# Kernel tuning notes

Measured on AMD Instinct MI355X. Metric: run time of the kernel, lower is better.

## Reference

```python
import jax, jax.numpy as jnp
import numpy as np

NUM_OBJECTS = 32  # instance ids 1..32; id 0 = background (skipped in original loop)


def setup_inputs() -> dict:
    key = jax.random.key(0)
    k0, k1, k2, k3 = jax.random.split(key, 4)
    B, C, H, W = 4, 256, 256, 256
    encoded = jax.random.normal(k0, (B, C, H, W), dtype=jnp.float32)
    # dense random ids 0..NUM_OBJECTS; with 65536 pixels every id appears w.h.p.
    masks = jax.random.randint(k1, (B, 1, H, W), 0, NUM_OBJECTS + 1, dtype=jnp.int32)
    w1 = jax.random.normal(k2, (C, C // 2), dtype=jnp.float32) * 0.02
    b1 = jnp.zeros((C // 2,), dtype=jnp.float32)
    w2 = jax.random.normal(k3, (C // 2, 4), dtype=jnp.float32) * 0.02
    b2 = jnp.zeros((4,), dtype=jnp.float32)
    return {"encoded": encoded, "w1": w1, "b1": b1, "w2": w2, "b2": b2, "masks": masks}


def reference(encoded, w1, b1, w2, b2, masks):
    # encoded: [B, C, H, W], masks: [B, 1, H, W] int ids in [0, NUM_OBJECTS]
    B, C, H, W = encoded.shape
    P = H * W
    ids = masks[:, 0].reshape(B, P)                      # [B, P]
    feat = encoded.reshape(B, C, P).transpose(0, 2, 1)   # [B, P, C]
    # Fused single-pass segmented max (replaces the per-id rescan loop).
    seg = jax.vmap(
        lambda d, i: jax.ops.segment_max(d, i, num_segments=NUM_OBJECTS + 1)
    )(feat, ids)                                          # [B, N+1, C]
    # Original computes max(mask * feat): zeros outside the mask participate in
    # the max, so the result is clamped at 0. Also fills any empty segment with 0.
    pooled = jnp.maximum(seg[:, 1:], 0.0)                 # [B, N, C] (drop background id 0)
    h = pooled @ w1 + b1                                  # [B, N, C//2]
    bbox = jax.nn.sigmoid(h @ w2 + b2)                    # [B, N, 4]
    return bbox
```

## Files before the change

kernel.cpp:

```cpp
#include <hip/hip_runtime.h>
#include <math.h>

#define BATCH   4
#define CH      256
#define PIX     65536
#define NIDS    33
#define NOBJ    32

__global__ __launch_bounds__(256, 1) void segmax_kernel(
    const float* __restrict__ encoded,
    const int*   __restrict__ masks,
    float*       __restrict__ pooled)
{
    __shared__ float smax[NIDS * 256];
    __shared__ float partial[NOBJ * 8];

    const int t   = threadIdx.x;
    const int bid = blockIdx.x;
    const int b   = bid >> 8;
    const int c   = bid & 255;

    #pragma unroll
    for (int i = 0; i < NIDS; ++i)
        smax[i * 256 + t] = -INFINITY;
    __syncthreads();

    const float4* __restrict__ vals = (const float4*)(encoded + (size_t)bid * PIX);
    const int4*   __restrict__ ids  = (const int4*)(masks + (size_t)b * PIX);

    #pragma unroll 2
    for (int it = 0; it < 64; ++it) {
        const int idx = it * 256 + t;
        const float4 v = vals[idx];
        const int4   m = ids[idx];
        { float* p = &smax[m.x * 256 + t]; *p = fmaxf(*p, v.x); }
        { float* p = &smax[m.y * 256 + t]; *p = fmaxf(*p, v.y); }
        { float* p = &smax[m.z * 256 + t]; *p = fmaxf(*p, v.z); }
        { float* p = &smax[m.w * 256 + t]; *p = fmaxf(*p, v.w); }
    }
    __syncthreads();

    {
        const int id   = 1 + (t >> 3);
        const int g    = t & 7;
        const int base = id * 256 + g * 32;
        float m = -INFINITY;
        #pragma unroll
        for (int j = 0; j < 32; ++j) {
            const int jj = (j + t) & 31;
            m = fmaxf(m, smax[base + jj]);
        }
        partial[(id - 1) * 8 + g] = m;
    }
    __syncthreads();

    if (t < NOBJ) {
        float m = -INFINITY;
        #pragma unroll
        for (int g = 0; g < 8; ++g) m = fmaxf(m, partial[t * 8 + g]);
        m = fmaxf(m, 0.0f);
        pooled[((size_t)b * NOBJ + t) * CH + c] = m;
    }
}

__global__ __launch_bounds__(128, 1) void mlp_kernel(
    const float* __restrict__ pooled,
    const float* __restrict__ w1, const float* __restrict__ b1,
    const float* __restrict__ w2, const float* __restrict__ b2,
    float*       __restrict__ out)
{
    __shared__ float row[CH];
    __shared__ float h[128];
    const int t = threadIdx.x;
    const int r = blockIdx.x;

    row[t]       = pooled[(size_t)r * CH + t];
    row[t + 128] = pooled[(size_t)r * CH + t + 128];
    __syncthreads();

    float acc = b1[t];
    #pragma unroll 8
    for (int i = 0; i < CH; ++i)
        acc = fmaf(row[i], w1[i * 128 + t], acc);
    h[t] = acc;
    __syncthreads();

    if (t < 4) {
        float a = b2[t];
        #pragma unroll 8
        for (int i = 0; i < 128; ++i)
            a = fmaf(h[i], w2[i * 4 + t], a);
        out[(size_t)r * 4 + t] = 1.0f / (1.0f + expf(-a));
    }
}

extern "C" void kernel_launch(void* const* d_in, const int* in_sizes, int n_in,
                              void* d_out, int out_size, void* d_ws, size_t ws_size,
                              hipStream_t stream) {
    const float* encoded = (const float*)d_in[0];
    const float* w1      = (const float*)d_in[1];
    const float* b1      = (const float*)d_in[2];
    const float* w2      = (const float*)d_in[3];
    const float* b2      = (const float*)d_in[4];
    const int*   masks   = (const int*)  d_in[5];
    float* out    = (float*)d_out;
    float* pooled = (float*)d_ws;

    segmax_kernel<<<BATCH * CH, 256, 0, stream>>>(encoded, masks, pooled);
    mlp_kernel<<<BATCH * NOBJ, 128, 0, stream>>>(pooled, w1, b1, w2, b2, out);
}
```

Before: 384.8 us.

## Pack mask ids to bytes, split pixel range across two blocks, prefetch loads

```diff
diff --git a/kernel.cpp b/kernel.cpp
--- a/kernel.cpp
+++ b/kernel.cpp
@@ -6,37 +6,62 @@
 #define PIX     65536
 #define NIDS    33
 #define NOBJ    32
+#define SSPLIT  2
+#define F4_SLICE (PIX / 4)
+#define F4_PER_S (F4_SLICE / SSPLIT)
+#define ITERS    (F4_PER_S / 256)
+
+typedef float f32x4 __attribute__((ext_vector_type(4)));
+
+__global__ __launch_bounds__(256) void pack_masks_kernel(
+    const int* __restrict__ masks, unsigned int* __restrict__ maskw)
+{
+    const int idx = blockIdx.x * 256 + threadIdx.x;
+    const int4 v = ((const int4*)masks)[idx];
+    maskw[idx] = (unsigned)v.x | ((unsigned)v.y << 8) |
+                 ((unsigned)v.z << 16) | ((unsigned)v.w << 24);
+}
 
 __global__ __launch_bounds__(256, 1) void segmax_kernel(
-    const float* __restrict__ encoded,
-    const int*   __restrict__ masks,
-    float*       __restrict__ pooled)
+    const float*        __restrict__ encoded,
+    const unsigned int* __restrict__ maskw,
+    float*              __restrict__ pooledP)
 {
     __shared__ float smax[NIDS * 256];
     __shared__ float partial[NOBJ * 8];
 
-    const int t   = threadIdx.x;
-    const int bid = blockIdx.x;
-    const int b   = bid >> 8;
-    const int c   = bid & 255;
+    const int t     = threadIdx.x;
+    const int slice = blockIdx.x >> 1;
+    const int s     = blockIdx.x & 1;
+    const int b     = slice >> 8;
+    const int c     = slice & 255;
 
     #pragma unroll
     for (int i = 0; i < NIDS; ++i)
         smax[i * 256 + t] = -INFINITY;
     __syncthreads();
 
-    const float4* __restrict__ vals = (const float4*)(encoded + (size_t)bid * PIX);
-    const int4*   __restrict__ ids  = (const int4*)(masks + (size_t)b * PIX);
+    const f32x4* __restrict__ vals =
+        (const f32x4*)encoded + (size_t)slice * F4_SLICE + (size_t)s * F4_PER_S;
+    const unsigned int* __restrict__ mw =
+        maskw + (size_t)b * F4_SLICE + (size_t)s * F4_PER_S;
 
-    #pragma unroll 2
-    for (int it = 0; it < 64; ++it) {
-        const int idx = it * 256 + t;
-        const float4 v = vals[idx];
-        const int4   m = ids[idx];
-        { float* p = &smax[m.x * 256 + t]; *p = fmaxf(*p, v.x); }
-        { float* p = &smax[m.y * 256 + t]; *p = fmaxf(*p, v.y); }
-        { float* p = &smax[m.z * 256 + t]; *p = fmaxf(*p, v.z); }
-        { float* p = &smax[m.w * 256 + t]; *p = fmaxf(*p, v.w); }
+    f32x4 v = __builtin_nontemporal_load(vals + t);
+    unsigned int m = mw[t];
+
+    #pragma unroll 4
+    for (int it = 0; it < ITERS; ++it) {
+        f32x4 nv;
+        unsigned int nm = 0;
+        if (it + 1 < ITERS) {
+            nv = __builtin_nontemporal_load(vals + (it + 1) * 256 + t);
+            nm = mw[(it + 1) * 256 + t];
+        }
+        { float* p = &smax[((m      ) & 255) * 256 + t]; *p = fmaxf(*p, v.x); }
+        { float* p = &smax[((m >>  8) & 255) * 256 + t]; *p = fmaxf(*p, v.y); }
+        { float* p = &smax[((m >> 16) & 255) * 256 + t]; *p = fmaxf(*p, v.z); }
+        { float* p = &smax[((m >> 24)      ) * 256 + t]; *p = fmaxf(*p, v.w); }
+        v = nv; m = nm;
     }
     __syncthreads();
 
@@ -44,45 +69,55 @@
         const int id   = 1 + (t >> 3);
         const int g    = t & 7;
         const int base = id * 256 + g * 32;
-        float m = -INFINITY;
+        float mx = -INFINITY;
         #pragma unroll
         for (int j = 0; j < 32; ++j) {
             const int jj = (j + t) & 31;
-            m = fmaxf(m, smax[base + jj]);
+            mx = fmaxf(mx, smax[base + jj]);
         }
-        partial[(id - 1) * 8 + g] = m;
+        partial[(id - 1) * 8 + g] = mx;
     }
     __syncthreads();
 
     if (t < NOBJ) {
-        float m = -INFINITY;
+        float mx = -INFINITY;
         #pragma unroll
-        for (int g = 0; g < 8; ++g) m = fmaxf(m, partial[t * 8 + g]);
-        m = fmaxf(m, 0.0f);
-        pooled[((size_t)b * NOBJ + t) * CH + c] = m;
+        for (int g = 0; g < 8; ++g) mx = fmaxf(mx, partial[t * 8 + g]);
+        pooledP[((size_t)s * BATCH * NOBJ + (size_t)b * NOBJ + t) * CH + c] = mx;
     }
 }
 
-__global__ __launch_bounds__(128, 1) void mlp_kernel(
-    const float* __restrict__ pooled,
+__global__ __launch_bounds__(256, 1) void mlp_kernel(
+    const float* __restrict__ pooledP,
     const float* __restrict__ w1, const float* __restrict__ b1,
     const float* __restrict__ w2, const float* __restrict__ b2,
     float*       __restrict__ out)
 {
     __shared__ float row[CH];
+    __shared__ float hpart[256];
     __shared__ float h[128];
     const int t = threadIdx.x;
     const int r = blockIdx.x;
 
-    row[t]       = pooled[(size_t)r * CH + t];
-    row[t + 128] = pooled[(size_t)r * CH + t + 128];
+    {
+        const float p0 = pooledP[(size_t)r * CH + t];
+        const float p1 = pooledP[((size_t)BATCH * NOBJ + r) * CH + t];
+        row[t] = fmaxf(fmaxf(p0, p1), 0.0f);
+    }
     __syncthreads();
 
-    float acc = b1[t];
-    #pragma unroll 8
-    for (int i = 0; i < CH; ++i)
-        acc = fmaf(row[i], w1[i * 128 + t], acc);
-    h[t] = acc;
+    {
+        const int j  = t & 127;
+        const int kh = t >> 7;
+        float acc = (kh == 0) ? b1[j] : 0.0f;
+        const int kbase = kh * 128;
+        #pragma unroll 8
+        for (int i = 0; i < 128; ++i)
+            acc = fmaf(row[kbase + i], w1[(kbase + i) * 128 + j], acc);
+        hpart[t] = acc;
+    }
+    __syncthreads();
+    if (t < 128) h[t] = hpart[t] + hpart[t + 128];
     __syncthreads();
 
     if (t < 4) {
@@ -103,9 +138,12 @@
     const float* w2      = (const float*)d_in[3];
     const float* b2      = (const float*)d_in[4];
     const int*   masks   = (const int*)  d_in[5];
-    float* out    = (float*)d_out;
-    float* pooled = (float*)d_ws;
+    float* out = (float*)d_out;
 
-    segmax_kernel<<<BATCH * CH, 256, 0, stream>>>(encoded, masks, pooled);
-    mlp_kernel<<<BATCH * NOBJ, 128, 0, stream>>>(pooled, w1, b1, w2, b2, out);
+    unsigned int* maskw  = (unsigned int*)d_ws;
+    float*        pooledP = (float*)d_ws + BATCH * F4_SLICE;
+
+    pack_masks_kernel<<<BATCH * PIX / 4 / 256, 256, 0, stream>>>(masks, maskw);
+    segmax_kernel<<<BATCH * CH * SSPLIT, 256, 0, stream>>>(encoded, maskw, pooledP);
+    mlp_kernel<<<BATCH * NOBJ, 256, 0, stream>>>(pooledP, w1, b1, w2, b2, out);
 }
```

New measurement: 356.8 us. -7.3%, faster.
